# Kernel tuning notes

Measured on AMD Instinct MI355X. Metric: run time of the kernel, lower is better.

## Reference

```python
import jax, jax.numpy as jnp
import numpy as np

N, E = 100000, 1600000
EPS = 1e-5  # BatchNorm1d default eps


def setup_inputs() -> dict:
    key = jax.random.key(0)
    ks = jax.random.split(key, 12)
    rn = lambda k, s, sc=0.05: jax.random.normal(k, s, dtype=jnp.float32) * sc
    return {
        "x": rn(ks[0], (N, 4), 1.0),
        "edge_attr": rn(ks[1], (E, 1), 1.0),
        "edge_index": jax.random.randint(ks[2], (2, E), 0, N),
        # Meta1 edge model: NNConv(9 -> 84) acting as a per-edge linear, + BN(84)
        "W_e1": rn(ks[3], (9, 84)), "b_e1": jnp.zeros((84,), jnp.float32),
        "g_bn1": jnp.ones((84,), jnp.float32), "be_bn1": jnp.zeros((84,), jnp.float32),
        # Meta1 node model: NNConv(88 -> 128) + BN(128), then Linear(132, 64)
        "W_n1": rn(ks[4], (88, 128)), "b_n1": jnp.zeros((128,), jnp.float32),
        "g_bn2": jnp.ones((128,), jnp.float32), "be_bn2": jnp.zeros((128,), jnp.float32),
        "W_m2": rn(ks[5], (132, 64)), "b_m2": jnp.zeros((64,), jnp.float32),
        # Meta2 edge model: Linear(212, 1)
        "W_e2": rn(ks[6], (212, 1)), "b_e2": jnp.zeros((1,), jnp.float32),
        # Meta2 node model: Linear(65, 4) (output discarded by the module)
        "W_n2": rn(ks[7], (65, 4)), "b_n2": jnp.zeros((4,), jnp.float32),
    }


def _batchnorm(h, g, b):
    # training-mode BatchNorm1d: batch mean / biased batch var
    m = jnp.mean(h, axis=0)
    v = jnp.mean(jnp.square(h - m), axis=0)
    return (h - m) * jax.lax.rsqrt(v + EPS) * g + b


def _scatter_mean(vals, idx, n):
    s = jax.ops.segment_sum(vals, idx, num_segments=n)
    cnt = jax.ops.segment_sum(jnp.ones((vals.shape[0],), vals.dtype), idx, num_segments=n)
    return s / jnp.maximum(cnt, 1.0)[:, None]


def reference(x, edge_attr, edge_index, W_e1, b_e1, g_bn1, be_bn1,
              W_n1, b_n1, g_bn2, be_bn2, W_m2, b_m2, W_e2, b_e2, W_n2, b_n2):
    row, col = edge_index[0], edge_index[1]
    n = x.shape[0]
    # --- Meta layer 1 ---
    # edge model: cat([src, dest, edge_attr]) -> NNConv(9,84) -> BN(84)
    e_in = jnp.concatenate([x[row], x[col], edge_attr], axis=1)            # [E, 9]
    e1 = _batchnorm(e_in @ W_e1 + b_e1, g_bn1, be_bn1)                     # [E, 84]
    # node model 1: gather + linear + BN + scatter_mean + concat + MLP
    h = jnp.concatenate([x[col], e1], axis=1) @ W_n1 + b_n1                # [E, 128]
    h = _batchnorm(h, g_bn2, be_bn2)
    agg = _scatter_mean(h, row, n)                                         # [N, 128]
    x1 = jax.nn.relu(jnp.concatenate([x, agg], axis=1) @ W_m2 + b_m2)      # [N, 64]
    # --- Meta layer 2 ---
    e2 = jax.nn.relu(
        jnp.concatenate([x1[row], x1[col], e1], axis=1) @ W_e2 + b_e2)     # [E, 1]
    # node model 2 is computed by the torch module but its output is discarded
    h2 = jax.nn.relu(jnp.concatenate([x1[col], e2], axis=1) @ W_n2 + b_n2)  # [E, 4]
    _x2 = jnp.concatenate([x1, _scatter_mean(h2, row, n)], axis=1)         # dead code
    return e2
```

## Files before the change

kernel.cpp:

```cpp
#include <hip/hip_runtime.h>


#define NBLK_A 512
#define M21 0x1FFFFFULL
#define QS2 2048.0f
#define QB2 16384

__global__ __launch_bounds__(256) void k_passA(
    const int* __restrict__ ei, const float* __restrict__ ea,
    int2* __restrict__ rec, int* __restrict__ len,
    int NB, int CAP, int shift, int SUBm, int E, int EPB)
{
    __shared__ int hist[256];
    int t = threadIdx.x;
    int blk = blockIdx.x;
    hist[t] = 0;
    __syncthreads();
    int e0 = blk * EPB;
    int e1 = min(E, e0 + EPB);
    size_t base = (size_t)blk * NB;
    for (int e = e0 + t; e < e1; e += 256) {
        int r = ei[e];
        int c = ei[E + e];
        float a = ea[e];
        int b = r >> shift;
        int slot = atomicAdd(&hist[b], 1);
        if (slot < CAP) {
            int w0 = c | ((r & SUBm) << 17);
            rec[(base + b) * CAP + slot] = make_int2(w0, __float_as_int(a));
        }
    }
    __syncthreads();
    if (t < NB) len[base + t] = min(hist[t], CAP);
}

template <int SUB, int CAPT>
__global__ __launch_bounds__(256) void k_passB(
    const int2* __restrict__ rec, const int* __restrict__ len,
    const float4* __restrict__ x4, unsigned long long* __restrict__ p,
    float* __restrict__ Up, int NB, int CH)
{
    __shared__ unsigned long long Sacc[SUB * 2];
    __shared__ int pre[65];
    __shared__ float red[16];
    int t = threadIdx.x;
    int b = blockIdx.x;
    int j = blockIdx.y;
    for (int k = t; k < SUB * 2; k += 256) Sacc[k] = 0ULL;
    int s0 = j * 64;
    if (t < 64) {
        int v = min(len[(size_t)(s0 + t) * NB + b], CAPT);
#pragma unroll
        for (int off = 1; off < 64; off <<= 1) {
            int w = __shfl_up(v, off);
            if (t >= off) v += w;
        }
        pre[t + 1] = v;
        if (t == 0) pre[0] = 0;
    }
    if (t < 16) red[t] = 0.f;
    __syncthreads();
    int R = pre[64];
    float u[15];
#pragma unroll
    for (int k = 0; k < 15; ++k) u[k] = 0.f;
#pragma unroll 4
    for (int idx = t; idx < R; idx += 256) {
        int lo = 0, hi = 64;
        while (hi - lo > 1) {
            int mid = (lo + hi) >> 1;
            if (pre[mid] <= idx) lo = mid; else hi = mid;
        }
        int slot = idx - pre[lo];
        int2 v = rec[((size_t)(s0 + lo) * NB + b) * CAPT + slot];
        int c = v.x & 0x1FFFF;
        int ridx = v.x >> 17;
        float a = __int_as_float(v.y);
        float4 xc = x4[c];
        int q0 = __float2int_rn(xc.x * QS2);
        int q1 = __float2int_rn(xc.y * QS2);
        int q2 = __float2int_rn(xc.z * QS2);
        int q3 = __float2int_rn(xc.w * QS2);
        int qa = __float2int_rn(a * QS2);
        q0 = min(max(q0, -16383), 16383);
        q1 = min(max(q1, -16383), 16383);
        q2 = min(max(q2, -16383), 16383);
        q3 = min(max(q3, -16383), 16383);
        qa = min(max(qa, -16383), 16383);
        unsigned long long w0 =
            (unsigned long long)(unsigned)(q0 + QB2) |
            ((unsigned long long)(unsigned)(q1 + QB2) << 21) |
            ((unsigned long long)(unsigned)(q2 + QB2) << 42);
        unsigned long long w1 =
            (unsigned long long)(unsigned)(q3 + QB2) |
            ((unsigned long long)(unsigned)(qa + QB2) << 21) |
            (1ULL << 42);
        atomicAdd(&Sacc[ridx * 2], w0);
        atomicAdd(&Sacc[ridx * 2 + 1], w1);
        float zc[4] = {xc.x, xc.y, xc.z, xc.w};
        int q = 0;
#pragma unroll
        for (int i = 0; i < 4; ++i)
#pragma unroll
            for (int k = i; k < 4; ++k) { u[q] = fmaf(zc[i], zc[k], u[q]); ++q; }
#pragma unroll
        for (int i = 0; i < 4; ++i) u[10 + i] = fmaf(zc[i], a, u[10 + i]);
        u[14] = fmaf(a, a, u[14]);
    }
    __syncthreads();
    float4* pb = (float4*)(p + (size_t)(b * CH + j) * (SUB * 2));
    const float4* sa = (const float4*)Sacc;
    for (int k = t; k < SUB; k += 256) pb[k] = sa[k];
    int lane = t & 63;
#pragma unroll
    for (int v = 0; v < 15; ++v) {
        float s = u[v];
#pragma unroll
        for (int off = 32; off > 0; off >>= 1) s += __shfl_down(s, off);
        if (lane == 0) atomicAdd(&red[v], s);
    }
    __syncthreads();
    if (t < 15) Up[(size_t)(b * CH + j) * 16 + t] = red[t];
}

__global__ __launch_bounds__(256) void k_reduce(
    const unsigned long long* __restrict__ p, const float4* __restrict__ x4,
    float* __restrict__ MSx, float* __restrict__ Tp,
    int N, int shift, int SUBm, int CH)
{
    __shared__ float red[40];
    int t = threadIdx.x;
    int n = blockIdx.x * 256 + t;
    float Tacc[39];
#pragma unroll
    for (int k = 0; k < 39; ++k) Tacc[k] = 0.f;
    if (n < N) {
        int b = n >> shift;
        int i = n & SUBm;
        int SUB = SUBm + 1;
        long long f0 = 0, f1 = 0, f2 = 0, f3 = 0, fa = 0, cn = 0;
        for (int j = 0; j < CH; ++j) {
            const unsigned long long* pb = p + (size_t)(b * CH + j) * (SUB * 2);
            unsigned long long w0 = pb[(size_t)i * 2];
            unsigned long long w1 = pb[(size_t)i * 2 + 1];
            f0 += (long long)(w0 & M21);
            f1 += (long long)((w0 >> 21) & M21);
            f2 += (long long)((w0 >> 42) & M21);
            f3 += (long long)(w1 & M21);
            fa += (long long)((w1 >> 21) & M21);
            cn += (long long)(w1 >> 42);
        }
        float cnt = (float)cn;
        long long bias = cn * (long long)QB2;
        float S[6];
        S[0] = (float)(f0 - bias) / QS2;
        S[1] = (float)(f1 - bias) / QS2;
        S[2] = (float)(f2 - bias) / QS2;
        S[3] = (float)(f3 - bias) / QS2;
        S[4] = (float)(fa - bias) / QS2;
        S[5] = cnt;
        float4 xn = x4[n];
        float x[4] = {xn.x, xn.y, xn.z, xn.w};
        int q = 0;
#pragma unroll
        for (int a = 0; a < 4; ++a)
#pragma unroll
            for (int bb = a; bb < 4; ++bb) { Tacc[q] = cnt * x[a] * x[bb]; ++q; }
#pragma unroll
        for (int a = 0; a < 4; ++a)
#pragma unroll
            for (int bb = 0; bb < 4; ++bb) Tacc[10 + a * 4 + bb] = x[a] * S[bb];
#pragma unroll
        for (int a = 0; a < 4; ++a) {
            Tacc[26 + a] = x[a] * S[4];
            Tacc[30 + a] = cnt * x[a];
            Tacc[34 + a] = S[a];
        }
        Tacc[38] = S[4];
        float inv = cnt > 0.f ? 1.f / cnt : 0.f;
        float4* m = (float4*)(MSx + (size_t)n * 8);
        m[0] = make_float4(S[0] * inv, S[1] * inv, S[2] * inv, S[3] * inv);
        m[1] = make_float4(S[4] * inv, cnt > 0.f ? 1.f : 0.f, 0.f, 0.f);
    }
    int lane = t & 63;
    if (t < 40) red[t] = 0.f;
    __syncthreads();
#pragma unroll
    for (int v = 0; v < 39; ++v) {
        float s = Tacc[v];
#pragma unroll
        for (int off = 32; off > 0; off >>= 1) s += __shfl_down(s, off);
        if (lane == 0) atomicAdd(&red[v], s);
    }
    __syncthreads();
    if (t < 39) Tp[(size_t)blockIdx.x * 40 + t] = red[t];
}

__device__ __forceinline__ int sym4(int a, int b) {
    return a * 4 - a * (a - 1) / 2 + (b - a);
}

__global__ __launch_bounds__(1024) void k_setup(
    const float* __restrict__ Up, const float* __restrict__ Tp,
    int NBu, int NTb,
    const float* __restrict__ We1, const float* __restrict__ be1,
    const float* __restrict__ g1, const float* __restrict__ bb1,
    const float* __restrict__ Wn1, const float* __restrict__ bn1,
    const float* __restrict__ g2, const float* __restrict__ bb2,
    const float* __restrict__ We2, const float* __restrict__ be2,
    const float* __restrict__ Wm2, const float* __restrict__ bm2,
    float* __restrict__ G, float* __restrict__ c0g, float* __restrict__ kvg,
    int E)
{
    __shared__ float ZCl[64];
    __shared__ float Zf[100];
    __shared__ float s1[84], sh1[84];
    __shared__ float Ml[10 * 128];
    __shared__ float s2l[128], sh2l[128];
    __shared__ float Ep[16 * 64 * 11];
    int t = threadIdx.x;
    int lane = t & 63;
    if (t < 64) ZCl[t] = 0.f;
    __syncthreads();
    {
        float us[15];
#pragma unroll
        for (int k = 0; k < 15; ++k) us[k] = 0.f;
        for (int i = t; i < NBu; i += 1024)
#pragma unroll
            for (int k = 0; k < 15; ++k) us[k] += Up[(size_t)i * 16 + k];
        float ts[39];
#pragma unroll
        for (int k = 0; k < 39; ++k) ts[k] = 0.f;
        for (int i = t; i < NTb; i += 1024)
#pragma unroll
            for (int k = 0; k < 39; ++k) ts[k] += Tp[(size_t)i * 40 + k];
#pragma unroll
        for (int v = 0; v < 15; ++v) {
            float s = us[v];
#pragma unroll
            for (int off = 32; off > 0; off >>= 1) s += __shfl_down(s, off);
            if (lane == 0) atomicAdd(&ZCl[39 + v], s);
        }
#pragma unroll
        for (int v = 0; v < 39; ++v) {
            float s = ts[v];
#pragma unroll
            for (int off = 32; off > 0; off >>= 1) s += __shfl_down(s, off);
            if (lane == 0) atomicAdd(&ZCl[v], s);
        }
    }
    __syncthreads();
    if (t < 100) {
        int i = t / 10, jj = t % 10;
        int a_ = i < jj ? i : jj;
        int b_ = i < jj ? jj : i;
        float v;
        if (b_ < 4) v = ZCl[sym4(a_, b_)];
        else if (b_ < 8) {
            if (a_ < 4) v = ZCl[10 + a_ * 4 + (b_ - 4)];
            else v = ZCl[39 + sym4(a_ - 4, b_ - 4)];
        } else if (b_ == 8) {
            if (a_ < 4) v = ZCl[26 + a_];
            else if (a_ < 8) v = ZCl[49 + (a_ - 4)];
            else v = ZCl[53];
        } else {
            if (a_ < 4) v = ZCl[30 + a_];
            else if (a_ < 8) v = ZCl[34 + (a_ - 4)];
            else if (a_ == 8) v = ZCl[38];
            else v = (float)E;
        }
        Zf[t] = v;
    }
    __syncthreads();
    float Ef = (float)E;
    if (t < 84) {
        float w[10];
#pragma unroll
        for (int i = 0; i < 9; ++i) w[i] = We1[i * 84 + t];
        w[9] = be1[t];
        float sm = 0.f, sq = 0.f;
#pragma unroll
        for (int i = 0; i < 10; ++i) {
            sm += Zf[90 + i] * w[i];
            float zi = 0.f;
#pragma unroll
            for (int jj = 0; jj < 10; ++jj) zi += Zf[i * 10 + jj] * w[jj];
            sq += w[i] * zi;
        }
        float m = sm / Ef;
        float var = sq / Ef - m * m;
        float sc = g1[t] * rsqrtf(var + 1e-5f);
        s1[t] = sc;
        sh1[t] = bb1[t] - m * sc;
    }
    __syncthreads();
    {
        int j = t & 127;
        int sub = t >> 7;
        float col[10];
#pragma unroll
        for (int i = 0; i < 10; ++i) col[i] = 0.f;
        int k0 = sub * 11;
        int k1 = min(84, k0 + 11);
        for (int k = k0; k < k1; ++k) {
            float wn = Wn1[(4 + k) * 128 + j];
            float ws_ = s1[k] * wn;
#pragma unroll
            for (int i = 0; i < 9; ++i) col[i] = fmaf(We1[i * 84 + k], ws_, col[i]);
            col[9] += be1[k] * ws_ + sh1[k] * wn;
        }
        float* bp = &Ep[(size_t)(sub * 128 + j) * 10];
#pragma unroll
        for (int i = 0; i < 10; ++i) bp[i] = col[i];
    }
    __syncthreads();
    if (t < 128) {
        float col[10];
#pragma unroll
        for (int i = 0; i < 10; ++i) col[i] = 0.f;
        for (int sub = 0; sub < 8; ++sub) {
            const float* bp = &Ep[(size_t)(sub * 128 + t) * 10];
#pragma unroll
            for (int i = 0; i < 10; ++i) col[i] += bp[i];
        }
#pragma unroll
        for (int i = 0; i < 4; ++i) col[4 + i] += Wn1[i * 128 + t];
        col[9] += bn1[t];
#pragma unroll
        for (int i = 0; i < 10; ++i) Ml[i * 128 + t] = col[i];
    }
    __syncthreads();
    if (t < 128) {
        float col[10];
#pragma unroll
        for (int i = 0; i < 10; ++i) col[i] = Ml[i * 128 + t];
        float sm = 0.f, sq = 0.f;
#pragma unroll
        for (int i = 0; i < 10; ++i) {
            sm += Zf[90 + i] * col[i];
            float zi = 0.f;
#pragma unroll
            for (int jj = 0; jj < 10; ++jj) zi += Zf[i * 10 + jj] * col[jj];
            sq += col[i] * zi;
        }
        float m = sm / Ef;
        float var = sq / Ef - m * m;
        float sc = g2[t] * rsqrtf(var + 1e-5f);
        s2l[t] = sc;
        sh2l[t] = bb2[t] - m * sc;
    } else if (t >= 128 && t < 768) {
        int col = (t - 128) >> 6;
        float kv = 0.f;
        if (col < 9) {
            for (int k = lane; k < 84; k += 64)
                kv = fmaf(We1[col * 84 + k] * s1[k], We2[128 + k], kv);
        } else {
            for (int k = lane; k < 84; k += 64)
                kv = fmaf(be1[k] * s1[k] + sh1[k], We2[128 + k], kv);
        }
#pragma unroll
        for (int off = 32; off > 0; off >>= 1) kv += __shfl_down(kv, off);
        if (lane == 0) kvg[col] = kv + (col == 9 ? be2[0] : 0.f);
    }
    __syncthreads();
    {
        int j = t & 63;
        int sub = t >> 6;
        float gcol[10];
#pragma unroll
        for (int i = 0; i < 10; ++i) gcol[i] = 0.f;
        float c0 = 0.f;
        int k0 = sub * 8;
        for (int k = k0; k < k0 + 8; ++k) {
            float bkj = Wm2[(4 + k) * 64 + j];
            float m = s2l[k] * bkj;
#pragma unroll
            for (int i = 0; i < 10; ++i) gcol[i] = fmaf(Ml[i * 128 + k], m, gcol[i]);
            c0 = fmaf(sh2l[k], bkj, c0);
        }
        float* ep = &Ep[(size_t)(sub * 64 + j) * 11];
#pragma unroll
        for (int i = 0; i < 10; ++i) ep[i] = gcol[i];
        ep[10] = c0;
    }
    __syncthreads();
    if (t < 64) {
        float gcol[10];
#pragma unroll
        for (int i = 0; i < 10; ++i) gcol[i] = 0.f;
        float c0 = 0.f;
        for (int sub = 0; sub < 16; ++sub) {
            const float* ep = &Ep[(size_t)(sub * 64 + t) * 11];
#pragma unroll
            for (int i = 0; i < 10; ++i) gcol[i] += ep[i];
            c0 += ep[10];
        }
#pragma unroll
        for (int i = 0; i < 4; ++i) gcol[i] += Wm2[i * 64 + t];
        c0 += bm2[t];
#pragma unroll
        for (int i = 0; i < 10; ++i) G[i * 64 + t] = gcol[i];
        c0g[t] = c0;
    }
}

__global__ __launch_bounds__(256) void k_nodesB(
    const float4* __restrict__ x4, const float* __restrict__ MSx,
    const float* __restrict__ G, const float* __restrict__ c0g,
    const float* __restrict__ kv, const float* __restrict__ Wm2,
    const float* __restrict__ bm2, const float* __restrict__ We2,
    float* __restrict__ P, float* __restrict__ Q, int N)
{
    __shared__ float Gl[640], c0l[64], Al[256], bl[64], ul[64], vl[64], kvl[10];
    int t = threadIdx.x;
    for (int k = t; k < 640; k += 256) Gl[k] = G[k];
    if (t < 64) {
        c0l[t] = c0g[t];
        bl[t] = bm2[t];
        ul[t] = We2[t];
        vl[t] = We2[64 + t];
    }
    for (int k = t; k < 256; k += 256) Al[k] = Wm2[k];
    if (t < 10) kvl[t] = kv[t];
    __syncthreads();
    int n = blockIdx.x * 256 + t;
    if (n >= N) return;
    float4 xn = x4[n];
    const float4* m = (const float4*)(MSx + (size_t)n * 8);
    float4 m0 = m[0];
    float4 m1 = m[1];
    bool has = m1.y > 0.5f;
    float Pv = 0.f, Qv = 0.f;
    if (has) {
        float zb[10] = {xn.x, xn.y, xn.z, xn.w, m0.x, m0.y, m0.z, m0.w, m1.x, 1.f};
#pragma unroll 4
        for (int j = 0; j < 64; ++j) {
            float s = c0l[j];
#pragma unroll
            for (int i = 0; i < 10; ++i) s = fmaf(zb[i], Gl[i * 64 + j], s);
            s = fmaxf(s, 0.f);
            Pv = fmaf(s, ul[j], Pv);
            Qv = fmaf(s, vl[j], Qv);
        }
    } else {
#pragma unroll 4
        for (int j = 0; j < 64; ++j) {
            float s = bl[j] + xn.x * Al[j] + xn.y * Al[64 + j] +
                      xn.z * Al[128 + j] + xn.w * Al[192 + j];
            s = fmaxf(s, 0.f);
            Pv = fmaf(s, ul[j], Pv);
            Qv = fmaf(s, vl[j], Qv);
        }
    }
    P[n] = Pv + xn.x * kvl[0] + xn.y * kvl[1] + xn.z * kvl[2] + xn.w * kvl[3];
    Q[n] = Qv + xn.x * kvl[4] + xn.y * kvl[5] + xn.z * kvl[6] + xn.w * kvl[7];
}

__global__ __launch_bounds__(256) void k_edges_out(
    const int* __restrict__ ei, const float* __restrict__ ea,
    const float* __restrict__ P, const float* __restrict__ Q,
    const float* __restrict__ kv, float* __restrict__ out, int E)
{
    int e2 = blockIdx.x * 256 + threadIdx.x;
    int e = e2 * 2;
    float k8 = kv[8], k9 = kv[9];
    if (e + 1 < E) {
        int2 rr = *(const int2*)&ei[e];
        int2 cc = *(const int2*)&ei[E + e];
        float2 aa = *(const float2*)&ea[e];
        float s0 = P[rr.x] + Q[cc.x] + aa.x * k8 + k9;
        float s1 = P[rr.y] + Q[cc.y] + aa.y * k8 + k9;
        float2 o;
        o.x = s0 > 0.f ? s0 : 0.f;
        o.y = s1 > 0.f ? s1 : 0.f;
        *(float2*)&out[e] = o;
    } else if (e < E) {
        float s = P[ei[e]] + Q[ei[E + e]] + ea[e] * k8 + k9;
        out[e] = s > 0.f ? s : 0.f;
    }
}

extern "C" void kernel_launch(void* const* d_in, const int* in_sizes, int n_in,
                              void* d_out, int out_size, void* d_ws, size_t ws_size,
                              hipStream_t stream)
{
    const float* x   = (const float*)d_in[0];
    const float* ea  = (const float*)d_in[1];
    const int*   ei  = (const int*)d_in[2];
    const float* We1 = (const float*)d_in[3];
    const float* be1 = (const float*)d_in[4];
    const float* g1  = (const float*)d_in[5];
    const float* bb1 = (const float*)d_in[6];
    const float* Wn1 = (const float*)d_in[7];
    const float* bn1 = (const float*)d_in[8];
    const float* g2  = (const float*)d_in[9];
    const float* bb2 = (const float*)d_in[10];
    const float* Wm2 = (const float*)d_in[11];
    const float* bm2 = (const float*)d_in[12];
    const float* We2 = (const float*)d_in[13];
    const float* be2 = (const float*)d_in[14];

    int N = in_sizes[0] / 4;
    int E = in_sizes[1];
    int EPB = (E + NBLK_A - 1) / NBLK_A;

    int NB    = (N + 1023) >> 10;
    int CAP   = 96;
    int CH    = 8;
    int shift = 10;
    int SUBm  = 1023;

    float* ws  = (float*)d_ws;
    float* G   = ws + 64;
    float* c0  = ws + 704;
    float* kv  = ws + 768;
    float* P   = ws + 1024;
    float* Q   = P + N;
    float* MSx = Q + N;
    int*   len = (int*)(MSx + 8 * (size_t)N);
    int2*  rec = (int2*)(len + (size_t)NBLK_A * NB);
    unsigned long long* prt =
        (unsigned long long*)(rec + (size_t)NBLK_A * NB * CAP);

    float* Up = P;
    float* Tp = P + 32768;
    int NBu = NB * CH;
    int NTb = (N + 255) / 256;

    k_passA<<<NBLK_A, 256, 0, stream>>>(ei, ea, rec, len, NB, CAP, shift,
                                        SUBm, E, EPB);
    k_passB<1024, 96><<<dim3(NB, CH), 256, 0, stream>>>(
        rec, len, (const float4*)x, prt, Up, NB, CH);
    k_reduce<<<NTb, 256, 0, stream>>>(prt, (const float4*)x, MSx, Tp, N,
                                      shift, SUBm, CH);
    k_setup<<<1, 1024, 0, stream>>>(Up, Tp, NBu, NTb, We1, be1, g1, bb1, Wn1,
                                    bn1, g2, bb2, We2, be2, Wm2, bm2, G, c0,
                                    kv, E);
    k_nodesB<<<(N + 255) / 256, 256, 0, stream>>>((const float4*)x, MSx, G,
                                                  c0, kv, Wm2, bm2, We2, P, Q,
                                                  N);
    k_edges_out<<<(E / 2 + 256) / 256, 256, 0, stream>>>(ei, ea, P, Q, kv,
                                                         (float*)d_out, E);
}
```

Measured before the change: 109.3 us.

## Fuse setup into reduce kernel via last-block-done atomic counter

Merges the single-block setup kernel into the per-node reduce kernel. Each block bumps a global counter after writing its partials, and the last block to finish runs the setup work with 256 threads instead of 1024. Loop partitions are rescaled to fit the smaller block. This removes one kernel launch and its gap, but the setup now runs serially on one 256-thread block at the tail, with fewer threads to spread the work.

```diff
diff --git a/kernel.cpp b/kernel.cpp
--- a/kernel.cpp
+++ b/kernel.cpp
@@ -8,12 +8,13 @@
 
 __global__ __launch_bounds__(256) void k_passA(
     const int* __restrict__ ei, const float* __restrict__ ea,
-    int2* __restrict__ rec, int* __restrict__ len,
+    int2* __restrict__ rec, int* __restrict__ len, int* __restrict__ done,
     int NB, int CAP, int shift, int SUBm, int E, int EPB)
 {
     __shared__ int hist[256];
     int t = threadIdx.x;
     int blk = blockIdx.x;
+    if (blk == 0 && t == 0) *done = 0;
     hist[t] = 0;
     __syncthreads();
     int e0 = blk * EPB;
@@ -123,12 +124,31 @@
     if (t < 15) Up[(size_t)(b * CH + j) * 16 + t] = red[t];
 }
 
-__global__ __launch_bounds__(256) void k_reduce(
+__device__ __forceinline__ int sym4(int a, int b) {
+    return a * 4 - a * (a - 1) / 2 + (b - a);
+}
+
+__global__ __launch_bounds__(256) void k_reduce_setup(
     const unsigned long long* __restrict__ p, const float4* __restrict__ x4,
-    float* __restrict__ MSx, float* __restrict__ Tp,
-    int N, int shift, int SUBm, int CH)
+    float* __restrict__ MSx, float* __restrict__ Tp, float* __restrict__ Up,
+    int* __restrict__ done, int N, int shift, int SUBm, int CH, int NBu,
+    const float* __restrict__ We1, const float* __restrict__ be1,
+    const float* __restrict__ g1, const float* __restrict__ bb1,
+    const float* __restrict__ Wn1, const float* __restrict__ bn1,
+    const float* __restrict__ g2, const float* __restrict__ bb2,
+    const float* __restrict__ We2, const float* __restrict__ be2,
+    const float* __restrict__ Wm2, const float* __restrict__ bm2,
+    float* __restrict__ G, float* __restrict__ c0g, float* __restrict__ kvg,
+    int E)
 {
     __shared__ float red[40];
+    __shared__ float ZCl[64];
+    __shared__ float Zf[100];
+    __shared__ float s1[84], sh1[84];
+    __shared__ float Ml[10 * 128];
+    __shared__ float s2l[128], sh2l[128];
+    __shared__ float Ep[2816];
+    __shared__ int lastFlag;
     int t = threadIdx.x;
     int n = blockIdx.x * 256 + t;
     float Tacc[39];
@@ -194,45 +214,28 @@
     }
     __syncthreads();
     if (t < 39) Tp[(size_t)blockIdx.x * 40 + t] = red[t];
-}
-
-__device__ __forceinline__ int sym4(int a, int b) {
-    return a * 4 - a * (a - 1) / 2 + (b - a);
-}
-
-__global__ __launch_bounds__(1024) void k_setup(
-    const float* __restrict__ Up, const float* __restrict__ Tp,
-    int NBu, int NTb,
-    const float* __restrict__ We1, const float* __restrict__ be1,
-    const float* __restrict__ g1, const float* __restrict__ bb1,
-    const float* __restrict__ Wn1, const float* __restrict__ bn1,
-    const float* __restrict__ g2, const float* __restrict__ bb2,
-    const float* __restrict__ We2, const float* __restrict__ be2,
-    const float* __restrict__ Wm2, const float* __restrict__ bm2,
-    float* __restrict__ G, float* __restrict__ c0g, float* __restrict__ kvg,
-    int E)
-{
-    __shared__ float ZCl[64];
-    __shared__ float Zf[100];
-    __shared__ float s1[84], sh1[84];
-    __shared__ float Ml[10 * 128];
-    __shared__ float s2l[128], sh2l[128];
-    __shared__ float Ep[16 * 64 * 11];
-    int t = threadIdx.x;
-    int lane = t & 63;
+    __threadfence();
+    if (t == 0) {
+        int prev = atomicAdd(done, 1);
+        lastFlag = (prev == (int)gridDim.x - 1) ? 1 : 0;
+    }
+    __syncthreads();
+    if (!lastFlag) return;
+    __threadfence();
+    int NTb = (int)gridDim.x;
     if (t < 64) ZCl[t] = 0.f;
     __syncthreads();
     {
         float us[15];
 #pragma unroll
         for (int k = 0; k < 15; ++k) us[k] = 0.f;
-        for (int i = t; i < NBu; i += 1024)
+        for (int i = t; i < NBu; i += 256)
 #pragma unroll
             for (int k = 0; k < 15; ++k) us[k] += Up[(size_t)i * 16 + k];
         float ts[39];
 #pragma unroll
         for (int k = 0; k < 39; ++k) ts[k] = 0.f;
-        for (int i = t; i < NTb; i += 1024)
+        for (int i = t; i < NTb; i += 256)
 #pragma unroll
             for (int k = 0; k < 39; ++k) ts[k] += Tp[(size_t)i * 40 + k];
 #pragma unroll
@@ -301,9 +304,8 @@
         float col[10];
 #pragma unroll
         for (int i = 0; i < 10; ++i) col[i] = 0.f;
-        int k0 = sub * 11;
-        int k1 = min(84, k0 + 11);
-        for (int k = k0; k < k1; ++k) {
+        int k0 = sub * 42;
+        for (int k = k0; k < k0 + 42; ++k) {
             float wn = Wn1[(4 + k) * 128 + j];
             float ws_ = s1[k] * wn;
 #pragma unroll
@@ -318,12 +320,8 @@
     if (t < 128) {
         float col[10];
 #pragma unroll
-        for (int i = 0; i < 10; ++i) col[i] = 0.f;
-        for (int sub = 0; sub < 8; ++sub) {
-            const float* bp = &Ep[(size_t)(sub * 128 + t) * 10];
-#pragma unroll
-            for (int i = 0; i < 10; ++i) col[i] += bp[i];
-        }
+        for (int i = 0; i < 10; ++i)
+            col[i] = Ep[(size_t)t * 10 + i] + Ep[(size_t)(128 + t) * 10 + i];
 #pragma unroll
         for (int i = 0; i < 4; ++i) col[4 + i] += Wn1[i * 128 + t];
         col[9] += bn1[t];
@@ -349,8 +347,9 @@
         float sc = g2[t] * rsqrtf(var + 1e-5f);
         s2l[t] = sc;
         sh2l[t] = bb2[t] - m * sc;
-    } else if (t >= 128 && t < 768) {
-        int col = (t - 128) >> 6;
+    }
+    __syncthreads();
+    for (int col = t >> 6; col < 10; col += 4) {
         float kv = 0.f;
         if (col < 9) {
             for (int k = lane; k < 84; k += 64)
@@ -371,8 +370,8 @@
 #pragma unroll
         for (int i = 0; i < 10; ++i) gcol[i] = 0.f;
         float c0 = 0.f;
-        int k0 = sub * 8;
-        for (int k = k0; k < k0 + 8; ++k) {
+        int k0 = sub * 32;
+        for (int k = k0; k < k0 + 32; ++k) {
             float bkj = Wm2[(4 + k) * 64 + j];
             float m = s2l[k] * bkj;
 #pragma unroll
@@ -390,7 +389,8 @@
 #pragma unroll
         for (int i = 0; i < 10; ++i) gcol[i] = 0.f;
         float c0 = 0.f;
-        for (int sub = 0; sub < 16; ++sub) {
+#pragma unroll
+        for (int sub = 0; sub < 4; ++sub) {
             const float* ep = &Ep[(size_t)(sub * 64 + t) * 11];
 #pragma unroll
             for (int i = 0; i < 10; ++i) gcol[i] += ep[i];
@@ -511,15 +511,16 @@
     int shift = 10;
     int SUBm  = 1023;
 
-    float* ws  = (float*)d_ws;
-    float* G   = ws + 64;
-    float* c0  = ws + 704;
-    float* kv  = ws + 768;
-    float* P   = ws + 1024;
-    float* Q   = P + N;
-    float* MSx = Q + N;
-    int*   len = (int*)(MSx + 8 * (size_t)N);
-    int2*  rec = (int2*)(len + (size_t)NBLK_A * NB);
+    float* ws   = (float*)d_ws;
+    float* G    = ws + 64;
+    float* c0   = ws + 704;
+    float* kv   = ws + 768;
+    int*   done = (int*)(ws + 1008);
+    float* P    = ws + 1024;
+    float* Q    = P + N;
+    float* MSx  = Q + N;
+    int*   len  = (int*)(MSx + 8 * (size_t)N);
+    int2*  rec  = (int2*)(len + (size_t)NBLK_A * NB);
     unsigned long long* prt =
         (unsigned long long*)(rec + (size_t)NBLK_A * NB * CAP);
 
@@ -528,15 +529,14 @@
     int NBu = NB * CH;
     int NTb = (N + 255) / 256;
 
-    k_passA<<<NBLK_A, 256, 0, stream>>>(ei, ea, rec, len, NB, CAP, shift,
-                                        SUBm, E, EPB);
+    k_passA<<<NBLK_A, 256, 0, stream>>>(ei, ea, rec, len, done, NB, CAP,
+                                        shift, SUBm, E, EPB);
     k_passB<1024, 96><<<dim3(NB, CH), 256, 0, stream>>>(
         rec, len, (const float4*)x, prt, Up, NB, CH);
-    k_reduce<<<NTb, 256, 0, stream>>>(prt, (const float4*)x, MSx, Tp, N,
-                                      shift, SUBm, CH);
-    k_setup<<<1, 1024, 0, stream>>>(Up, Tp, NBu, NTb, We1, be1, g1, bb1, Wn1,
-                                    bn1, g2, bb2, We2, be2, Wm2, bm2, G, c0,
-                                    kv, E);
+    k_reduce_setup<<<NTb, 256, 0, stream>>>(
+        prt, (const float4*)x, MSx, Tp, Up, done, N, shift, SUBm, CH, NBu,
+        We1, be1, g1, bb1, Wn1, bn1, g2, bb2, We2, be2, Wm2, bm2, G, c0, kv,
+        E);
     k_nodesB<<<(N + 255) / 256, 256, 0, stream>>>((const float4*)x, MSx, G,
                                                   c0, kv, Wm2, bm2, We2, P, Q,
                                                   N);
```

Result: slower. 132.7 us (+21.4%).
